# Optimization experiments

Measured on AMD Instinct MI355X. Metric: run time of the kernel, lower is better.

## Reference

```python
import jax, jax.numpy as jnp
import numpy as np

N_EMBD = 768
N_HEAD = 12
HEAD_DIM = N_EMBD // N_HEAD


def setup_inputs() -> dict:
    key = jax.random.key(0)
    k1, k2, k3 = jax.random.split(key, 3)
    B, T, C = 4, 2048, N_EMBD
    x = jax.random.normal(k1, (B, T, C), dtype=jnp.float32)
    # c_attn: torch Linear(C, 3C) -> store as (C, 3C) for x @ W
    w_attn = jax.random.normal(k2, (C, 3 * C), dtype=jnp.float32) * (1.0 / np.sqrt(C))
    b_attn = jax.random.normal(k3, (3 * C,), dtype=jnp.float32) * 0.02
    return {"x": x, "w_attn": w_attn, "b_attn": b_attn}


def reference(x, w_attn, b_attn):
    B, T, C = x.shape
    H, D = N_HEAD, HEAD_DIM
    scale = 1.0 / np.sqrt(D).astype(np.float32)

    qkv = x @ w_attn + b_attn                      # (B, T, 3C)
    q, k, v = jnp.split(qkv, 3, axis=-1)
    q = q.reshape(B, T, H, D).transpose(0, 2, 1, 3)  # (B, H, T, D)
    k = k.reshape(B, T, H, D).transpose(0, 2, 1, 3)
    v = v.reshape(B, T, H, D).transpose(0, 2, 1, 3)

    att = jnp.einsum('bhid,bhjd->bhij', q, k) * scale  # (B, H, T, T)
    causal = jnp.tril(jnp.ones((T, T), dtype=bool))
    # masked positions -> -inf -> relu -> 0; kept positions -> relu(scaled score)
    att = jnp.where(causal, jnp.maximum(att, 0.0), 0.0)

    y = jnp.einsum('bhij,bhjd->bhid', att, v)      # (B, H, T, D)
    y = y.transpose(0, 2, 1, 3).reshape(B, T, C)
    return y
```

## Files before the change

kernel.cpp:

```cpp
#include <hip/hip_runtime.h>
#include <hip/hip_bf16.h>

typedef short bf16x8 __attribute__((ext_vector_type(8)));
typedef float f32x4  __attribute__((ext_vector_type(4)));
typedef unsigned short u16x4 __attribute__((ext_vector_type(4)));

#define CDIM   768
#define NQKV   2304
#define MROWS  8192
#define TSEQ   2048
#define HD     64
#define NHEAD  12
#define BHTOT  48

__device__ __forceinline__ unsigned short f2bf(float f) {
    unsigned int x;
    __builtin_memcpy(&x, &f, 4);
    unsigned int r = (x + 0x7fffu + ((x >> 16) & 1u)) >> 16;
    return (unsigned short)r;
}

__device__ __forceinline__ unsigned int pkbf(float a, float b) {
    unsigned int ua, ub;
    __builtin_memcpy(&ua, &a, 4);
    __builtin_memcpy(&ub, &b, 4);
    return __builtin_amdgcn_perm(ua + 0x8000u, ub + 0x8000u, 0x03020706u);
}

__device__ __forceinline__ f32x4 mfma16(bf16x8 a, bf16x8 b, f32x4 c) {
    return __builtin_amdgcn_mfma_f32_16x16x32_bf16(a, b, c, 0, 0, 0);
}

__device__ __forceinline__ void gl_lds16(const unsigned short* g, unsigned short* l) {
    __builtin_amdgcn_global_load_lds(
        (__attribute__((address_space(1))) void*)(g),
        (__attribute__((address_space(3))) void*)(l),
        16, 0, 0);
}

__global__ __launch_bounds__(256) void prep(
    const float* __restrict__ X, const float* __restrict__ W,
    unsigned short* __restrict__ Xb, unsigned short* __restrict__ Wt)
{
    const int tid = threadIdx.x, blk = blockIdx.x;
    if (blk < 432) {
        __shared__ __align__(16) unsigned short tile[64][72];
        const int bx = blk % 36, by = blk / 36;
#pragma unroll
        for (int c = 0; c < 4; c++) {
            int chunk = tid + 256 * c;
            int r = chunk >> 4, cc = chunk & 15;
            f32x4 v = *(const f32x4*)(W + (size_t)(by * 64 + r) * NQKV + bx * 64 + cc * 4);
#pragma unroll
            for (int j = 0; j < 4; j++) tile[cc * 4 + j][r] = f2bf(v[j]);
        }
        __syncthreads();
#pragma unroll
        for (int c = 0; c < 2; c++) {
            int chunk = tid + 256 * c;
            int r = chunk >> 3, cc = chunk & 7;
            bf16x8 v;
#pragma unroll
            for (int j = 0; j < 8; j++) v[j] = (short)tile[r][cc * 8 + j];
            *(bf16x8*)(Wt + (size_t)(bx * 64 + r) * CDIM + by * 64 + cc * 8) = v;
        }
    }
    for (size_t i4 = (size_t)blk * 256 + tid; i4 < (size_t)(MROWS * CDIM / 4);
         i4 += (size_t)448 * 256) {
        f32x4 v = *(const f32x4*)(X + i4 * 4);
        u16x4 o;
#pragma unroll
        for (int j = 0; j < 4; j++) o[j] = f2bf(v[j]);
        *(u16x4*)(Xb + i4 * 4) = o;
    }
}

#define BK 64

__global__ __launch_bounds__(512, 4) void qkv_gemm(
    const unsigned short* __restrict__ X,
    const unsigned short* __restrict__ Wt,
    const float* __restrict__ Bias,
    unsigned short* __restrict__ Q,
    unsigned short* __restrict__ Km,
    unsigned short* __restrict__ Vt)
{
    __shared__ __align__(16) unsigned short As[256 * BK];
    __shared__ __align__(16) unsigned short Bs[128 * BK];
    const int tid  = threadIdx.x;
    const int wave = tid >> 6, lane = tid & 63;
    const int quad = lane >> 4, m16 = lane & 15;
    const int wr = wave >> 1, wc = wave & 1;

    const int t   = blockIdx.x;
    const int xcd = t & 7, s = t >> 3;
    const int m0  = (xcd * 4 + (s & 3)) * 256;
    const int n0  = (s >> 2) * 128;

    f32x4 acc[4][4];
#pragma unroll
    for (int i = 0; i < 4; i++)
#pragma unroll
        for (int j = 0; j < 4; j++) acc[i][j] = f32x4{0.f, 0.f, 0.f, 0.f};

    const unsigned short* xb = X + (size_t)m0 * CDIM;
    const unsigned short* wb = Wt + (size_t)n0 * CDIM;

    const int spos = lane & 7;
    const int rb = m16 & 7;
    int arow[4], brow[2];
#pragma unroll
    for (int c = 0; c < 4; c++) arow[c] = (wave * 256 + c * 64 + lane) >> 3;
#pragma unroll
    for (int c = 0; c < 2; c++) brow[c] = (wave * 128 + c * 64 + lane) >> 3;

    for (int k0 = 0; k0 < CDIM; k0 += BK) {
#pragma unroll
        for (int c = 0; c < 4; c++) {
            int row = arow[c], ch = spos ^ (row & 7);
            gl_lds16(xb + (size_t)row * CDIM + k0 + ch * 8, As + wave * 2048 + c * 512);
        }
#pragma unroll
        for (int c = 0; c < 2; c++) {
            int row = brow[c], ch = spos ^ (row & 7);
            gl_lds16(wb + (size_t)row * CDIM + k0 + ch * 8, Bs + wave * 1024 + c * 512);
        }
        __syncthreads();
#pragma unroll
        for (int ks = 0; ks < 2; ks++) {
            bf16x8 af[4], bfg[4];
#pragma unroll
            for (int u = 0; u < 4; u++) {
                int rowa = wr * 64 + u * 16 + m16;
                int rowb = wc * 64 + u * 16 + m16;
                int pos = (ks * 4 + quad) ^ rb;
                af[u]  = *(const bf16x8*)(As + rowa * 64 + pos * 8);
                bfg[u] = *(const bf16x8*)(Bs + rowb * 64 + pos * 8);
            }
#pragma unroll
            for (int i = 0; i < 4; i++)
#pragma unroll
                for (int j = 0; j < 4; j++)
                    acc[i][j] = mfma16(af[i], bfg[j], acc[i][j]);
        }
        __syncthreads();
    }

    const int region = n0 / CDIM;
    const float qscale = (region == 0) ? 0.125f : 1.0f;
#pragma unroll
    for (int i = 0; i < 4; i++) {
        int row = m0 + wr * 64 + i * 16 + quad * 4;
#pragma unroll
        for (int j = 0; j < 4; j++) {
            int gcol = n0 + wc * 64 + j * 16 + m16;
            int cc = gcol - region * CDIM;
            int h = cc >> 6, d = cc & 63;
            float bv = Bias[gcol];
#pragma unroll
            for (int r = 0; r < 4; r++) {
                int gm = row + r;
                int b = gm >> 11, tq = gm & 2047;
                int bh = b * NHEAD + h;
                unsigned short o = f2bf((acc[i][j][r] + bv) * qscale);
                if (region == 0)      Q[((size_t)bh * TSEQ + tq) * HD + d] = o;
                else if (region == 1) Km[((size_t)bh * TSEQ + tq) * HD + d] = o;
                else                  Vt[((size_t)bh * HD + d) * TSEQ + tq] = o;
            }
        }
    }
}

#define LDSK 0
#define LDSV 8192

__global__ __launch_bounds__(256, 4) void attn(
    const unsigned short* __restrict__ Q,
    const unsigned short* __restrict__ Kmat,
    const unsigned short* __restrict__ Vt,
    float* __restrict__ Out)
{
    __shared__ __align__(16) unsigned short S[16384];

    const int tid  = threadIdx.x;
    const int wave = tid >> 6, lane = tid & 63;
    const int q4 = lane >> 4, m16 = lane & 15;
    const int q8 = m16 >> 2, m3 = m16 & 3;

    const int xcd = blockIdx.x & 7;
    const int idx = blockIdx.x >> 3;
    const int bh  = xcd * 6 + (idx % 6);
    const int it  = 15 - (idx / 6);
    const int i0  = it * 128;

    const unsigned short* qb = Q    + (size_t)bh * TSEQ * HD;
    const unsigned short* kb = Kmat + (size_t)bh * TSEQ * HD;
    const unsigned short* vb = Vt   + (size_t)bh * HD * TSEQ;

    bf16x8 qf[2][2];
#pragma unroll
    for (int si = 0; si < 2; si++)
#pragma unroll
        for (int ks = 0; ks < 2; ks++)
            qf[si][ks] = *(const bf16x8*)(qb +
                (size_t)(i0 + wave * 32 + si * 16 + m16) * HD + ks * 32 + q4 * 8);

    f32x4 oacc[2][4];
#pragma unroll
    for (int si = 0; si < 2; si++)
#pragma unroll
        for (int dn = 0; dn < 4; dn++) oacc[si][dn] = f32x4{0.f, 0.f, 0.f, 0.f};

    const int fr  = ((q8 & 1) << 2) | m3;
    const int kx0 = (q4 ^ fr) * 8;
    const int kx1 = kx0 ^ 32;
    const int krb = (q8 * 8 + m3) * 64;

    for (int jt = 0; jt <= it; jt++) {
        const int j0 = jt * 128;
#pragma unroll
        for (int cc = 0; cc < 4; cc++) {
            int cs = wave * 4 + cc;
            int rowK = cs * 8 + (lane >> 3);
            int chK  = (lane & 7) ^ ((((rowK >> 3) & 1) << 2) | (rowK & 3));
            gl_lds16(kb + (size_t)(j0 + rowK) * HD + chK * 8, &S[LDSK] + cs * 512);
        }
#pragma unroll
        for (int cc = 0; cc < 4; cc++) {
            int cs = wave * 4 + cc;
            int dV  = cs * 4 + (lane >> 4);
            int chV = (m16 & 8) | ((m16 ^ dV) & 7);
            gl_lds16(vb + (size_t)dV * TSEQ + j0 + chV * 8, &S[LDSV] + cs * 512);
        }
        asm volatile("s_waitcnt vmcnt(4)" ::: "memory");
        __builtin_amdgcn_s_barrier();

        const bool diag = (jt == it);

        unsigned int pk[4][2][2][2];
#pragma unroll
        for (int kk = 0; kk < 4; kk++) {
            const int kb0 = kk * 2048 + krb;
            bf16x8 kf_e0 = *(const bf16x8*)(&S[LDSK] + kb0 + kx0);
            bf16x8 kf_e1 = *(const bf16x8*)(&S[LDSK] + kb0 + kx1);
            bf16x8 kf_o0 = *(const bf16x8*)(&S[LDSK] + kb0 + 256 + kx0);
            bf16x8 kf_o1 = *(const bf16x8*)(&S[LDSK] + kb0 + 256 + kx1);

            f32x4 sacc[2][2];
#pragma unroll
            for (int o = 0; o < 2; o++)
#pragma unroll
                for (int si = 0; si < 2; si++) sacc[o][si] = f32x4{0.f, 0.f, 0.f, 0.f};
#pragma unroll
            for (int si = 0; si < 2; si++) {
                sacc[0][si] = mfma16(kf_e0, qf[si][0], sacc[0][si]);
                sacc[0][si] = mfma16(kf_e1, qf[si][1], sacc[0][si]);
                sacc[1][si] = mfma16(kf_o0, qf[si][0], sacc[1][si]);
                sacc[1][si] = mfma16(kf_o1, qf[si][1], sacc[1][si]);
            }

#pragma unroll
            for (int o = 0; o < 2; o++)
#pragma unroll
                for (int si = 0; si < 2; si++) {
                    f32x4 v = sacc[o][si];
                    if (diag) {
#pragma unroll
                        for (int r = 0; r < 4; r++) {
                            int gj = kk * 32 + q4 * 8 + o * 4 + r;
                            int gi = wave * 32 + si * 16 + m16;
                            if (gj > gi) v[r] = 0.f;
                        }
                    }
#pragma unroll
                    for (int r = 0; r < 4; r++) v[r] = fmaxf(v[r], 0.f);
                    pk[kk][o][si][0] = pkbf(v[0], v[1]);
                    pk[kk][o][si][1] = pkbf(v[2], v[3]);
                }
        }

        asm volatile("s_waitcnt vmcnt(0)" ::: "memory");
        __builtin_amdgcn_s_barrier();

#pragma unroll
        for (int kk = 0; kk < 4; kk++) {
#pragma unroll
            for (int dn = 0; dn < 4; dn++) {
                int vsw = ((kk * 4 + q4) ^ (m16 & 7)) * 8;
                bf16x8 vf = *(const bf16x8*)(&S[LDSV] + (dn * 16 + m16) * 128 + vsw);
#pragma unroll
                for (int si = 0; si < 2; si++) {
                    union { bf16x8 v; unsigned int u[4]; } af;
                    af.u[0] = pk[kk][0][si][0];
                    af.u[1] = pk[kk][0][si][1];
                    af.u[2] = pk[kk][1][si][0];
                    af.u[3] = pk[kk][1][si][1];
                    oacc[si][dn] = mfma16(af.v, vf, oacc[si][dn]);
                }
            }
        }
        asm volatile("s_waitcnt lgkmcnt(0)" ::: "memory");
        __builtin_amdgcn_s_barrier();
    }

    const int b = bh / NHEAD, h = bh % NHEAD;
#pragma unroll
    for (int si = 0; si < 2; si++) {
        int ri = i0 + wave * 32 + si * 16 + q4 * 4;
#pragma unroll
        for (int dn = 0; dn < 4; dn++) {
            int d = dn * 16 + m16;
#pragma unroll
            for (int r = 0; r < 4; r++) {
                Out[((size_t)b * TSEQ + ri + r) * CDIM + h * HD + d] = oacc[si][dn][r];
            }
        }
    }
}

extern "C" void kernel_launch(void* const* d_in, const int* in_sizes, int n_in,
                              void* d_out, int out_size, void* d_ws, size_t ws_size,
                              hipStream_t stream) {
    const float* X    = (const float*)d_in[0];
    const float* W    = (const float*)d_in[1];
    const float* Bias = (const float*)d_in[2];
    float* out = (float*)d_out;

    unsigned short* Xb = (unsigned short*)d_ws;
    unsigned short* Wt = Xb + (size_t)MROWS * CDIM;
    unsigned short* Q  = Wt + (size_t)NQKV * CDIM;
    unsigned short* Km = Q  + (size_t)BHTOT * TSEQ * HD;
    unsigned short* Vt = Km + (size_t)BHTOT * TSEQ * HD;

    hipLaunchKernelGGL(prep, dim3(448), dim3(256), 0, stream, X, W, Xb, Wt);
    hipLaunchKernelGGL(qkv_gemm, dim3(576), dim3(512), 0, stream,
                       Xb, Wt, Bias, Q, Km, Vt);
    hipLaunchKernelGGL(attn, dim3(BHTOT * 16), dim3(256), 0, stream, Q, Km, Vt, out);
}
```

Baseline: 181.6 us.

## Double attention query tile to 256 rows with 512-thread blocks sharing K/V tiles

The attention kernel now processes 256 query rows per block with 8 waves instead of 128 rows with 4, so each K/V tile loaded into LDS is reused by twice as many waves and half as many blocks are launched. Each wave loads half as many K/V chunks, and waves whose rows lie entirely above the causal diagonal skip compute with a live flag while still taking part in barriers. Sched barriers pin the ordering of instructions around the syncs. The cost is coarser load balancing, fewer blocks in the grid, and idle waves on the diagonal tiles.

After: 217.5 us. 19.7% more time.

```diff
diff --git a/kernel.cpp b/kernel.cpp
--- a/kernel.cpp
+++ b/kernel.cpp
@@ -174,7 +174,7 @@
 #define LDSK 0
 #define LDSV 8192
 
-__global__ __launch_bounds__(256, 4) void attn(
+__global__ __launch_bounds__(512, 4) void attn(
     const unsigned short* __restrict__ Q,
     const unsigned short* __restrict__ Kmat,
     const unsigned short* __restrict__ Vt,
@@ -190,8 +190,10 @@
     const int xcd = blockIdx.x & 7;
     const int idx = blockIdx.x >> 3;
     const int bh  = xcd * 6 + (idx % 6);
-    const int it  = 15 - (idx / 6);
-    const int i0  = it * 128;
+    const int itv = 7 - (idx / 6);
+    const int i0  = itv * 256;
+    const int i0w = i0 + wave * 32;
+    const int jtmax = 2 * itv + 1;
 
     const unsigned short* qb = Q    + (size_t)bh * TSEQ * HD;
     const unsigned short* kb = Kmat + (size_t)bh * TSEQ * HD;
@@ -203,7 +205,7 @@
 #pragma unroll
         for (int ks = 0; ks < 2; ks++)
             qf[si][ks] = *(const bf16x8*)(qb +
-                (size_t)(i0 + wave * 32 + si * 16 + m16) * HD + ks * 32 + q4 * 8);
+                (size_t)(i0w + si * 16 + m16) * HD + ks * 32 + q4 * 8);
 
     f32x4 oacc[2][4];
 #pragma unroll
@@ -216,97 +218,109 @@
     const int kx1 = kx0 ^ 32;
     const int krb = (q8 * 8 + m3) * 64;
 
-    for (int jt = 0; jt <= it; jt++) {
+    int ksrow[2], kschk[2], vsrow[2], vschk[2];
+#pragma unroll
+    for (int cc = 0; cc < 2; cc++) {
+        int cs = wave * 2 + cc;
+        ksrow[cc] = cs * 8 + (lane >> 3);
+        kschk[cc] = (lane & 7) ^ ((((ksrow[cc] >> 3) & 1) << 2) | (ksrow[cc] & 3));
+        vsrow[cc] = cs * 4 + (lane >> 4);
+        vschk[cc] = (m16 & 8) | ((m16 ^ vsrow[cc]) & 7);
+    }
+
+    for (int jt = 0; jt <= jtmax; jt++) {
         const int j0 = jt * 128;
 #pragma unroll
-        for (int cc = 0; cc < 4; cc++) {
-            int cs = wave * 4 + cc;
-            int rowK = cs * 8 + (lane >> 3);
-            int chK  = (lane & 7) ^ ((((rowK >> 3) & 1) << 2) | (rowK & 3));
-            gl_lds16(kb + (size_t)(j0 + rowK) * HD + chK * 8, &S[LDSK] + cs * 512);
-        }
-#pragma unroll
-        for (int cc = 0; cc < 4; cc++) {
-            int cs = wave * 4 + cc;
-            int dV  = cs * 4 + (lane >> 4);
-            int chV = (m16 & 8) | ((m16 ^ dV) & 7);
-            gl_lds16(vb + (size_t)dV * TSEQ + j0 + chV * 8, &S[LDSV] + cs * 512);
-        }
-        asm volatile("s_waitcnt vmcnt(4)" ::: "memory");
+        for (int cc = 0; cc < 2; cc++)
+            gl_lds16(kb + (size_t)(j0 + ksrow[cc]) * HD + kschk[cc] * 8,
+                     &S[LDSK] + (wave * 2 + cc) * 512);
+#pragma unroll
+        for (int cc = 0; cc < 2; cc++)
+            gl_lds16(vb + (size_t)vsrow[cc] * TSEQ + j0 + vschk[cc] * 8,
+                     &S[LDSV] + (wave * 2 + cc) * 512);
+        asm volatile("s_waitcnt vmcnt(2)" ::: "memory");
         __builtin_amdgcn_s_barrier();
-
-        const bool diag = (jt == it);
+        __builtin_amdgcn_sched_barrier(0);
+
+        const bool live = (j0 <= i0w + 31);
+        const bool diag = live && (j0 + 127 > i0w);
 
         unsigned int pk[4][2][2][2];
-#pragma unroll
-        for (int kk = 0; kk < 4; kk++) {
-            const int kb0 = kk * 2048 + krb;
-            bf16x8 kf_e0 = *(const bf16x8*)(&S[LDSK] + kb0 + kx0);
-            bf16x8 kf_e1 = *(const bf16x8*)(&S[LDSK] + kb0 + kx1);
-            bf16x8 kf_o0 = *(const bf16x8*)(&S[LDSK] + kb0 + 256 + kx0);
-            bf16x8 kf_o1 = *(const bf16x8*)(&S[LDSK] + kb0 + 256 + kx1);
-
-            f32x4 sacc[2][2];
-#pragma unroll
-            for (int o = 0; o < 2; o++)
-#pragma unroll
-                for (int si = 0; si < 2; si++) sacc[o][si] = f32x4{0.f, 0.f, 0.f, 0.f};
-#pragma unroll
-            for (int si = 0; si < 2; si++) {
-                sacc[0][si] = mfma16(kf_e0, qf[si][0], sacc[0][si]);
-                sacc[0][si] = mfma16(kf_e1, qf[si][1], sacc[0][si]);
-                sacc[1][si] = mfma16(kf_o0, qf[si][0], sacc[1][si]);
-                sacc[1][si] = mfma16(kf_o1, qf[si][1], sacc[1][si]);
-            }
-
-#pragma unroll
-            for (int o = 0; o < 2; o++)
+        if (live) {
+#pragma unroll
+            for (int kk = 0; kk < 4; kk++) {
+                const int kb0 = kk * 2048 + krb;
+                bf16x8 kf_e0 = *(const bf16x8*)(&S[LDSK] + kb0 + kx0);
+                bf16x8 kf_e1 = *(const bf16x8*)(&S[LDSK] + kb0 + kx1);
+                bf16x8 kf_o0 = *(const bf16x8*)(&S[LDSK] + kb0 + 256 + kx0);
+                bf16x8 kf_o1 = *(const bf16x8*)(&S[LDSK] + kb0 + 256 + kx1);
+
+                f32x4 sacc[2][2];
+#pragma unroll
+                for (int o = 0; o < 2; o++)
+#pragma unroll
+                    for (int si = 0; si < 2; si++) sacc[o][si] = f32x4{0.f, 0.f, 0.f, 0.f};
 #pragma unroll
                 for (int si = 0; si < 2; si++) {
-                    f32x4 v = sacc[o][si];
-                    if (diag) {
-#pragma unroll
-                        for (int r = 0; r < 4; r++) {
-                            int gj = kk * 32 + q4 * 8 + o * 4 + r;
-                            int gi = wave * 32 + si * 16 + m16;
-                            if (gj > gi) v[r] = 0.f;
+                    sacc[0][si] = mfma16(kf_e0, qf[si][0], sacc[0][si]);
+                    sacc[0][si] = mfma16(kf_e1, qf[si][1], sacc[0][si]);
+                    sacc[1][si] = mfma16(kf_o0, qf[si][0], sacc[1][si]);
+                    sacc[1][si] = mfma16(kf_o1, qf[si][1], sacc[1][si]);
+                }
+
+#pragma unroll
+                for (int o = 0; o < 2; o++)
+#pragma unroll
+                    for (int si = 0; si < 2; si++) {
+                        f32x4 v = sacc[o][si];
+                        if (diag) {
+#pragma unroll
+                            for (int r = 0; r < 4; r++) {
+                                int gj = j0 + kk * 32 + q4 * 8 + o * 4 + r;
+                                int gi = i0w + si * 16 + m16;
+                                if (gj > gi) v[r] = 0.f;
+                            }
                         }
+#pragma unroll
+                        for (int r = 0; r < 4; r++) v[r] = fmaxf(v[r], 0.f);
+                        pk[kk][o][si][0] = pkbf(v[0], v[1]);
+                        pk[kk][o][si][1] = pkbf(v[2], v[3]);
                     }
-#pragma unroll
-                    for (int r = 0; r < 4; r++) v[r] = fmaxf(v[r], 0.f);
-                    pk[kk][o][si][0] = pkbf(v[0], v[1]);
-                    pk[kk][o][si][1] = pkbf(v[2], v[3]);
-                }
+            }
         }
 
         asm volatile("s_waitcnt vmcnt(0)" ::: "memory");
         __builtin_amdgcn_s_barrier();
-
-#pragma unroll
-        for (int kk = 0; kk < 4; kk++) {
-#pragma unroll
-            for (int dn = 0; dn < 4; dn++) {
-                int vsw = ((kk * 4 + q4) ^ (m16 & 7)) * 8;
-                bf16x8 vf = *(const bf16x8*)(&S[LDSV] + (dn * 16 + m16) * 128 + vsw);
-#pragma unroll
-                for (int si = 0; si < 2; si++) {
-                    union { bf16x8 v; unsigned int u[4]; } af;
-                    af.u[0] = pk[kk][0][si][0];
-                    af.u[1] = pk[kk][0][si][1];
-                    af.u[2] = pk[kk][1][si][0];
-                    af.u[3] = pk[kk][1][si][1];
-                    oacc[si][dn] = mfma16(af.v, vf, oacc[si][dn]);
+        __builtin_amdgcn_sched_barrier(0);
+
+        if (live) {
+#pragma unroll
+            for (int kk = 0; kk < 4; kk++) {
+#pragma unroll
+                for (int dn = 0; dn < 4; dn++) {
+                    int vsw = ((kk * 4 + q4) ^ (m16 & 7)) * 8;
+                    bf16x8 vf = *(const bf16x8*)(&S[LDSV] + (dn * 16 + m16) * 128 + vsw);
+#pragma unroll
+                    for (int si = 0; si < 2; si++) {
+                        union { bf16x8 v; unsigned int u[4]; } af;
+                        af.u[0] = pk[kk][0][si][0];
+                        af.u[1] = pk[kk][0][si][1];
+                        af.u[2] = pk[kk][1][si][0];
+                        af.u[3] = pk[kk][1][si][1];
+                        oacc[si][dn] = mfma16(af.v, vf, oacc[si][dn]);
+                    }
                 }
             }
         }
         asm volatile("s_waitcnt lgkmcnt(0)" ::: "memory");
         __builtin_amdgcn_s_barrier();
+        __builtin_amdgcn_sched_barrier(0);
     }
 
     const int b = bh / NHEAD, h = bh % NHEAD;
 #pragma unroll
     for (int si = 0; si < 2; si++) {
-        int ri = i0 + wave * 32 + si * 16 + q4 * 4;
+        int ri = i0w + si * 16 + q4 * 4;
 #pragma unroll
         for (int dn = 0; dn < 4; dn++) {
             int d = dn * 16 + m16;
@@ -335,5 +349,5 @@
     hipLaunchKernelGGL(prep, dim3(448), dim3(256), 0, stream, X, W, Xb, Wt);
     hipLaunchKernelGGL(qkv_gemm, dim3(576), dim3(512), 0, stream,
                        Xb, Wt, Bias, Q, Km, Vt);
-    hipLaunchKernelGGL(attn, dim3(BHTOT * 16), dim3(256), 0, stream, Q, Km, Vt, out);
-}
+    hipLaunchKernelGGL(attn, dim3(BHTOT * 8), dim3(512), 0, stream, Q, Km, Vt, out);
+}
```

## Double-buffer K in LDS, load V directly to registers, rebalance causal tile order

Applied to the files above, without the earlier changes.

The attention kernel now double-buffers K tiles in shared memory and prefetches the next K tile while the PV MFMAs run. The V operand is loaded straight from global memory into registers instead of staging it in LDS, which removes one barrier per iteration. The block-to-tile mapping is changed to interleave long and short causal rows for better load balance. The cost is many more vector registers for V (occupancy hint lowered from 4 to 3) and uncoalesced per-lane V loads.

New measurement: 213.6 us. 1.18x slower.

```diff
diff --git a/kernel.cpp b/kernel.cpp
--- a/kernel.cpp
+++ b/kernel.cpp
@@ -171,10 +171,7 @@
     }
 }
 
-#define LDSK 0
-#define LDSV 8192
-
-__global__ __launch_bounds__(256, 4) void attn(
+__global__ __launch_bounds__(256, 3) void attn(
     const unsigned short* __restrict__ Q,
     const unsigned short* __restrict__ Kmat,
     const unsigned short* __restrict__ Vt,
@@ -189,8 +186,10 @@
 
     const int xcd = blockIdx.x & 7;
     const int idx = blockIdx.x >> 3;
-    const int bh  = xcd * 6 + (idx % 6);
-    const int it  = 15 - (idx / 6);
+    const int p = idx & 31, g = idx >> 5;
+    const int r = (g == 0) ? p : ((g == 1) ? 95 - p : 32 + p);
+    const int bh  = xcd * 6 + (r % 6);
+    const int it  = 15 - (r / 6);
     const int i0  = it * 128;
 
     const unsigned short* qb = Q    + (size_t)bh * TSEQ * HD;
@@ -216,24 +215,34 @@
     const int kx1 = kx0 ^ 32;
     const int krb = (q8 * 8 + m3) * 64;
 
+    int ksrow[4], kschk[4];
+#pragma unroll
+    for (int cc = 0; cc < 4; cc++) {
+        int cs = wave * 4 + cc;
+        ksrow[cc] = cs * 8 + (lane >> 3);
+        kschk[cc] = (lane & 7) ^ ((((ksrow[cc] >> 3) & 1) << 2) | (ksrow[cc] & 3));
+    }
+
+#pragma unroll
+    for (int cc = 0; cc < 4; cc++)
+        gl_lds16(kb + (size_t)ksrow[cc] * HD + kschk[cc] * 8,
+                 S + (wave * 4 + cc) * 512);
+
     for (int jt = 0; jt <= it; jt++) {
         const int j0 = jt * 128;
-#pragma unroll
-        for (int cc = 0; cc < 4; cc++) {
-            int cs = wave * 4 + cc;
-            int rowK = cs * 8 + (lane >> 3);
-            int chK  = (lane & 7) ^ ((((rowK >> 3) & 1) << 2) | (rowK & 3));
-            gl_lds16(kb + (size_t)(j0 + rowK) * HD + chK * 8, &S[LDSK] + cs * 512);
-        }
-#pragma unroll
-        for (int cc = 0; cc < 4; cc++) {
-            int cs = wave * 4 + cc;
-            int dV  = cs * 4 + (lane >> 4);
-            int chV = (m16 & 8) | ((m16 ^ dV) & 7);
-            gl_lds16(vb + (size_t)dV * TSEQ + j0 + chV * 8, &S[LDSV] + cs * 512);
-        }
-        asm volatile("s_waitcnt vmcnt(4)" ::: "memory");
+        const unsigned short* Kb = S + (jt & 1) * 8192;
+
+        bf16x8 vreg[16];
+#pragma unroll
+        for (int kk = 0; kk < 4; kk++)
+#pragma unroll
+            for (int dn = 0; dn < 4; dn++)
+                vreg[kk * 4 + dn] = *(const bf16x8*)(vb +
+                    (size_t)(dn * 16 + m16) * TSEQ + j0 + kk * 32 + q4 * 8);
+
+        asm volatile("s_waitcnt vmcnt(16)" ::: "memory");
         __builtin_amdgcn_s_barrier();
+        __builtin_amdgcn_sched_barrier(0);
 
         const bool diag = (jt == it);
 
@@ -241,10 +250,10 @@
 #pragma unroll
         for (int kk = 0; kk < 4; kk++) {
             const int kb0 = kk * 2048 + krb;
-            bf16x8 kf_e0 = *(const bf16x8*)(&S[LDSK] + kb0 + kx0);
-            bf16x8 kf_e1 = *(const bf16x8*)(&S[LDSK] + kb0 + kx1);
-            bf16x8 kf_o0 = *(const bf16x8*)(&S[LDSK] + kb0 + 256 + kx0);
-            bf16x8 kf_o1 = *(const bf16x8*)(&S[LDSK] + kb0 + 256 + kx1);
+            bf16x8 kf_e0 = *(const bf16x8*)(Kb + kb0 + kx0);
+            bf16x8 kf_e1 = *(const bf16x8*)(Kb + kb0 + kx1);
+            bf16x8 kf_o0 = *(const bf16x8*)(Kb + kb0 + 256 + kx0);
+            bf16x8 kf_o1 = *(const bf16x8*)(Kb + kb0 + 256 + kx1);
 
             f32x4 sacc[2][2];
 #pragma unroll
@@ -266,28 +275,31 @@
                     f32x4 v = sacc[o][si];
                     if (diag) {
 #pragma unroll
-                        for (int r = 0; r < 4; r++) {
-                            int gj = kk * 32 + q4 * 8 + o * 4 + r;
+                        for (int rr = 0; rr < 4; rr++) {
+                            int gj = kk * 32 + q4 * 8 + o * 4 + rr;
                             int gi = wave * 32 + si * 16 + m16;
-                            if (gj > gi) v[r] = 0.f;
+                            if (gj > gi) v[rr] = 0.f;
                         }
                     }
 #pragma unroll
-                    for (int r = 0; r < 4; r++) v[r] = fmaxf(v[r], 0.f);
+                    for (int rr = 0; rr < 4; rr++) v[rr] = fmaxf(v[rr], 0.f);
                     pk[kk][o][si][0] = pkbf(v[0], v[1]);
                     pk[kk][o][si][1] = pkbf(v[2], v[3]);
                 }
         }
 
-        asm volatile("s_waitcnt vmcnt(0)" ::: "memory");
-        __builtin_amdgcn_s_barrier();
+        {
+            const int jn = (jt < it) ? (j0 + 128) : j0;
+#pragma unroll
+            for (int cc = 0; cc < 4; cc++)
+                gl_lds16(kb + (size_t)(jn + ksrow[cc]) * HD + kschk[cc] * 8,
+                         S + ((jt & 1) ^ 1) * 8192 + (wave * 4 + cc) * 512);
+        }
 
 #pragma unroll
         for (int kk = 0; kk < 4; kk++) {
 #pragma unroll
             for (int dn = 0; dn < 4; dn++) {
-                int vsw = ((kk * 4 + q4) ^ (m16 & 7)) * 8;
-                bf16x8 vf = *(const bf16x8*)(&S[LDSV] + (dn * 16 + m16) * 128 + vsw);
 #pragma unroll
                 for (int si = 0; si < 2; si++) {
                     union { bf16x8 v; unsigned int u[4]; } af;
@@ -295,12 +307,10 @@
                     af.u[1] = pk[kk][0][si][1];
                     af.u[2] = pk[kk][1][si][0];
                     af.u[3] = pk[kk][1][si][1];
-                    oacc[si][dn] = mfma16(af.v, vf, oacc[si][dn]);
+                    oacc[si][dn] = mfma16(af.v, vreg[kk * 4 + dn], oacc[si][dn]);
                 }
             }
         }
-        asm volatile("s_waitcnt lgkmcnt(0)" ::: "memory");
-        __builtin_amdgcn_s_barrier();
     }
 
     const int b = bh / NHEAD, h = bh % NHEAD;
@@ -311,8 +321,8 @@
         for (int dn = 0; dn < 4; dn++) {
             int d = dn * 16 + m16;
 #pragma unroll
-            for (int r = 0; r < 4; r++) {
-                Out[((size_t)b * TSEQ + ri + r) * CDIM + h * HD + d] = oacc[si][dn][r];
+            for (int rr = 0; rr < 4; rr++) {
+                Out[((size_t)b * TSEQ + ri + rr) * CDIM + h * HD + d] = oacc[si][dn][rr];
             }
         }
     }
```
